# Kernel tuning notes

Measured on AMD Instinct MI355X. Metric: run time of the kernel, lower is better.

## Reference

```python
import jax, jax.numpy as jnp
import numpy as np

B, W, D, R = 8, 1024, 1024, 64
GAMMA_MIN, GAMMA_MAX, ALPHA_CAP, EPS = 0.15, 1.0, 1.0, 1e-8


def _linear_init(key, fan_in, shape):
    bound = 1.0 / np.sqrt(fan_in)
    return jax.random.uniform(key, shape, jnp.float32, -bound, bound)


def setup_inputs() -> dict:
    key = jax.random.key(0)
    ks = jax.random.split(key, 12)
    h = jax.random.normal(ks[0], (B, W, D), jnp.float32)
    # k_base init as in __init__: exp(-0.15*max(j-i,0)) * tril, row-normalized
    pos = jnp.arange(W, dtype=jnp.float32)
    dist_ji = jnp.clip(pos[None, :] - pos[:, None], 0.0)
    causal = jnp.tril(jnp.ones((W, W), jnp.float32))
    k_init = jnp.exp(-0.15 * dist_ji) * causal
    k_base = k_init / jnp.clip(k_init.sum(axis=1, keepdims=True), 1e-8)
    # decay_logit init: gammas in [0.95, 0.995] -> inverse sigmoid of normalized gamma
    gammas = jnp.linspace(0.95, 0.995, R)
    graw = jnp.clip((gammas - GAMMA_MIN) / (GAMMA_MAX - GAMMA_MIN), 1e-6, 1 - 1e-6)
    decay_logit = jnp.log(graw / (1.0 - graw))
    return {
        "h": h,
        "k_base": k_base,
        "decay_logit": decay_logit,
        "gate_logit": jnp.asarray(8.0, jnp.float32),
        "alpha_logit": jnp.asarray(0.0, jnp.float32),
        "u": 0.05 * jax.random.normal(ks[1], (D, R), jnp.float32),
        "v": 0.05 * jax.random.normal(ks[2], (D, R), jnp.float32),
        "proj_w": _linear_init(ks[3], D, (D, D)),
        "proj_b": _linear_init(ks[4], D, (D,)),
        "norm1_scale": jnp.ones((D,), jnp.float32),
        "norm2_scale": jnp.ones((D,), jnp.float32),
        "up_w": _linear_init(ks[5], D, (2 * D, D)),
        "up_b": _linear_init(ks[6], D, (2 * D,)),
        "down_w": _linear_init(ks[7], 2 * D, (D, 2 * D)),
        "down_b": _linear_init(ks[8], 2 * D, (D,)),
    }


def _rmsnorm(x, scale):
    return x * jax.lax.rsqrt(jnp.mean(x * x, axis=-1, keepdims=True) + 1e-8) * scale


def _l2norm(x):
    # mirrors F.normalize(x, dim=-1, eps=1e-8)
    n = jnp.sqrt(jnp.sum(x * x, axis=-1, keepdims=True))
    return x / jnp.maximum(n, EPS)


def reference(h, k_base, decay_logit, gate_logit, alpha_logit, u, v,
              proj_w, proj_b, norm1_scale, norm2_scale,
              up_w, up_b, down_w, down_b):
    _, w, _ = h.shape
    pos = jnp.arange(w, dtype=h.dtype)
    causal = jnp.tril(jnp.ones((w, w), h.dtype))          # [W, W]
    dist = jnp.clip(pos[:, None] - pos[None, :], 0.0)     # i - j, clamped >= 0

    residual = h
    h_norm = _rmsnorm(h, norm1_scale)

    # dense k_base path (k_base_rank == 0)
    gate = jax.nn.sigmoid(gate_logit)
    kb = k_base[:w, :w] * causal
    out = gate * jnp.einsum('ij,bjd->bid', kb, h_norm)

    # low-rank q/k with per-rank gamma decay (decay_impl='mask')
    qk = h_norm @ jnp.concatenate((u, v), axis=1)          # [B, W, 2R]
    q_raw, k_raw = jnp.split(qk, [u.shape[1]], axis=-1)
    q = _l2norm(q_raw)
    k = _l2norm(k_raw)

    gamma = GAMMA_MIN + (GAMMA_MAX - GAMMA_MIN) * jax.nn.sigmoid(decay_logit)  # [R]
    log_gamma = jnp.log(jnp.clip(gamma, 1e-8))
    decay_mask = jnp.exp(dist[:, :, None] * log_gamma[None, None, :]) * causal[:, :, None]  # [W, W, R]

    alpha = ALPHA_CAP * jax.nn.sigmoid(alpha_logit)
    # scores[b,i,j] = sum_r q[b,i,r] * decay[i,j,r] * k[b,j,r]
    scores = jnp.einsum('bir,ijr,bjr->bij', q, decay_mask, k)
    out = out + alpha * jnp.einsum('bij,bjd->bid', scores, h_norm)

    h1 = residual + (out @ proj_w.T + proj_b)
    # MLP (GELU exact, mult=2), second residual
    m = _rmsnorm(h1, norm2_scale)
    m = jax.nn.gelu(m @ up_w.T + up_b, approximate=False) @ down_w.T + down_b
    return h1 + m
```

## Files before the change

kernel.cpp:

```cpp
#include <hip/hip_runtime.h>
#include <hip/hip_bf16.h>
#include <math.h>

#define B_ 8
#define W_ 1024
#define D_ 1024
#define R_ 64

typedef __hip_bfloat16 bf16;
typedef __attribute__((ext_vector_type(8))) short bf16x8;
typedef __attribute__((ext_vector_type(4))) float f32x4;

__device__ __forceinline__ float tof(bf16 x) { return __bfloat162float(x); }
__device__ __forceinline__ short f2bs(float f) {
    bf16 b = __float2bfloat16(f);
    return *(short*)&b;
}

__device__ __forceinline__ void async16(const void* g, void* l) {
    __builtin_amdgcn_global_load_lds(
        (const __attribute__((address_space(1))) unsigned int*)g,
        (__attribute__((address_space(3))) unsigned int*)l,
        16, 0, 0);
}

__global__ __launch_bounds__(256)
void rmsnorm_kernel(const float* __restrict__ src, const float* __restrict__ scale,
                    bf16* __restrict__ dst) {
    int row = blockIdx.x;
    const float* x = src + (size_t)row * D_;
    bf16* y = dst + (size_t)row * D_;
    float xv[4];
    float ss = 0.f;
#pragma unroll
    for (int it = 0; it < 4; ++it) {
        int d = threadIdx.x + it * 256;
        xv[it] = x[d];
        ss += xv[it] * xv[it];
    }
#pragma unroll
    for (int off = 32; off; off >>= 1) ss += __shfl_down(ss, off, 64);
    __shared__ float red[4];
    __shared__ float invs;
    int lane = threadIdx.x & 63, wid = threadIdx.x >> 6;
    if (lane == 0) red[wid] = ss;
    __syncthreads();
    if (threadIdx.x == 0) {
        float t = red[0] + red[1] + red[2] + red[3];
        invs = rsqrtf(t / (float)D_ + 1e-8f);
    }
    __syncthreads();
    float inv = invs;
#pragma unroll
    for (int it = 0; it < 4; ++it) {
        int d = threadIdx.x + it * 256;
        y[d] = __float2bfloat16(xv[it] * inv * scale[d]);
    }
}

__global__ __launch_bounds__(256)
void transpose_kernel(const bf16* __restrict__ src, bf16* __restrict__ dst) {
    int b = blockIdx.z;
    int j0 = blockIdx.x * 64, d0 = blockIdx.y * 64;
    __shared__ short Ts[64][72];
    const bf16* S = src + (size_t)b * W_ * D_;
    bf16* Dd = dst + (size_t)b * W_ * D_;
    int tid = threadIdx.x;
    int r = tid >> 3, c = (tid & 7) * 8;
#pragma unroll
    for (int p = 0; p < 2; ++p) {
        int j = r + p * 32;
        bf16x8 vv = *(const bf16x8*)&S[(size_t)(j0 + j) * D_ + d0 + c];
#pragma unroll
        for (int e = 0; e < 8; ++e) Ts[j][c + e] = vv[e];
    }
    __syncthreads();
#pragma unroll
    for (int p = 0; p < 2; ++p) {
        int d = r + p * 32;
        bf16x8 vv;
#pragma unroll
        for (int e = 0; e < 8; ++e) vv[e] = Ts[c + e][d];
        *(bf16x8*)&Dd[(size_t)(d0 + d) * W_ + j0 + c] = vv;
    }
}

__global__ __launch_bounds__(256)
void uvT_kernel(const float* __restrict__ u, const float* __restrict__ v,
                bf16* __restrict__ uvT) {
    int g = blockIdx.z;
    int d0 = blockIdx.x * 64;
    const float* src = g ? v : u;
    __shared__ float Ts[64][65];
    int tid = threadIdx.x;
#pragma unroll
    for (int e = 0; e < 16; ++e) {
        int idx = tid + e * 256;
        int drow = idx >> 6, rcol = idx & 63;
        Ts[drow][rcol] = src[(size_t)(d0 + drow) * 64 + rcol];
    }
    __syncthreads();
#pragma unroll
    for (int e = 0; e < 16; ++e) {
        int idx = tid + e * 256;
        int orow = idx >> 6, ocol = idx & 63;
        uvT[(size_t)(g * 64 + orow) * D_ + d0 + ocol] = __float2bfloat16(Ts[ocol][orow]);
    }
}

__global__ __launch_bounds__(256)
void convert3_kernel(const float* __restrict__ proj, const float* __restrict__ up,
                     const float* __restrict__ down,
                     bf16* __restrict__ projb, bf16* __restrict__ upb,
                     bf16* __restrict__ downb) {
    size_t idx = ((size_t)blockIdx.x * 256 + threadIdx.x) * 8;
    const size_t DD = (size_t)D_ * D_;
    const float* src; bf16* dst; size_t off;
    if (idx < DD)          { src = proj; dst = projb; off = idx; }
    else if (idx < 3 * DD) { src = up;   dst = upb;   off = idx - DD; }
    else                   { src = down; dst = downb; off = idx - 3 * DD; }
    float4 f0 = *(const float4*)(src + off);
    float4 f1 = *(const float4*)(src + off + 4);
    bf16x8 p;
    p[0] = f2bs(f0.x); p[1] = f2bs(f0.y); p[2] = f2bs(f0.z); p[3] = f2bs(f0.w);
    p[4] = f2bs(f1.x); p[5] = f2bs(f1.y); p[6] = f2bs(f1.z); p[7] = f2bs(f1.w);
    *(bf16x8*)(dst + off) = p;
}

__global__ __launch_bounds__(128)
void qk_epilogue_kernel(const float* __restrict__ qkraw,
                        const float* __restrict__ decay_logit,
                        float* __restrict__ qg, float* __restrict__ kg) {
    int row = blockIdx.x;
    int i = row & (W_ - 1);
    int t = threadIdx.x;
    int r = t & 63;
    bool isK = t >= 64;
    const size_t PS = (size_t)B_ * W_ * 128;
    size_t off = (size_t)row * 128 + t;
    float val = qkraw[off] + qkraw[PS + off] + qkraw[2 * PS + off] + qkraw[3 * PS + off];
    float sq = val * val;
#pragma unroll
    for (int o = 32; o; o >>= 1) sq += __shfl_xor(sq, o, 64);
    val = val / fmaxf(sqrtf(sq), 1e-8f);

    float dl = decay_logit[r];
    float gamma = 0.15f + 0.85f * (1.f / (1.f + expf(-dl)));
    float lg = logf(gamma);
    float e = isK ? expf(-(float)i * lg) : expf((float)i * lg);
    float o = val * e;
    if (isK) kg[(size_t)row * R_ + r] = o;
    else     qg[(size_t)row * R_ + r] = o;
}

__global__ __launch_bounds__(256)
void buildM_kernel(const float* __restrict__ qg, const float* __restrict__ kg,
                   const float* __restrict__ k_base,
                   const float* __restrict__ gate_logit,
                   const float* __restrict__ alpha_logit,
                   bf16* __restrict__ M) {
    int b = blockIdx.z;
    int ti = blockIdx.y, tj = blockIdx.x;
    int i0 = ti * 32, j0 = tj * 32;
    int tx = threadIdx.x, ty = threadIdx.y;
    bf16* Mb = M + (size_t)b * W_ * W_;
    const bf16 zero = __float2bfloat16(0.f);

    if (tj > ti) {
#pragma unroll
        for (int a = 0; a < 2; ++a)
#pragma unroll
            for (int c = 0; c < 2; ++c)
                Mb[(size_t)(i0 + ty * 2 + a) * W_ + (j0 + tx * 2 + c)] = zero;
        return;
    }

    __shared__ float Qs[32][65];
    __shared__ float Ks[32][65];
    int tid = ty * 16 + tx;
    for (int e = tid; e < 32 * 64; e += 256) {
        int rr = e & 63, row = e >> 6;
        Qs[row][rr] = qg[((size_t)b * W_ + i0 + row) * R_ + rr];
        Ks[row][rr] = kg[((size_t)b * W_ + j0 + row) * R_ + rr];
    }
    __syncthreads();

    float acc[2][2] = {{0.f, 0.f}, {0.f, 0.f}};
#pragma unroll 8
    for (int r = 0; r < 64; ++r) {
        float qa = Qs[ty * 2 + 0][r], qb = Qs[ty * 2 + 1][r];
        float ka = Ks[tx * 2 + 0][r], kb = Ks[tx * 2 + 1][r];
        acc[0][0] += qa * ka; acc[0][1] += qa * kb;
        acc[1][0] += qb * ka; acc[1][1] += qb * kb;
    }

    float gate  = 1.f / (1.f + expf(-(*gate_logit)));
    float alpha = 1.f / (1.f + expf(-(*alpha_logit)));
#pragma unroll
    for (int a = 0; a < 2; ++a) {
#pragma unroll
        for (int c = 0; c < 2; ++c) {
            int i = i0 + ty * 2 + a, j = j0 + tx * 2 + c;
            float vkb = k_base[(size_t)i * W_ + j];
            float out = (j <= i) ? (gate * vkb + alpha * acc[a][c]) : 0.f;
            Mb[(size_t)i * W_ + j] = __float2bfloat16(out);
        }
    }
}

#define BAR() do { __builtin_amdgcn_sched_barrier(0); \
                   __builtin_amdgcn_s_barrier(); \
                   __builtin_amdgcn_sched_barrier(0); } while (0)

__device__ __forceinline__ void mfma8(const bf16x8 (&fa)[2], const bf16x8 (&fb)[4],
                                      f32x4 (&acc)[2][4]) {
#pragma unroll
    for (int mi = 0; mi < 2; ++mi)
#pragma unroll
        for (int ni = 0; ni < 4; ++ni)
            acc[mi][ni] = __builtin_amdgcn_mfma_f32_16x16x32_bf16(
                fa[mi], fb[ni], acc[mi][ni], 0, 0, 0);
}

__device__ __forceinline__ void readf(const short* At0, const short* Bt0, int slot,
                                      const int (&ao)[2], const int (&bo)[4],
                                      bf16x8 (&fa)[2], bf16x8 (&fb)[4]) {
    const short* Ard = At0 + slot * 4096;
    const short* Brd = Bt0 + slot * 4096;
#pragma unroll
    for (int mi = 0; mi < 2; ++mi) fa[mi] = *(const bf16x8*)&Ard[ao[mi]];
#pragma unroll
    for (int ni = 0; ni < 4; ++ni) fb[ni] = *(const bf16x8*)&Brd[bo[ni]];
}

__device__ __forceinline__ void mfma16(const bf16x8 (&fa)[4], const bf16x8 (&fb)[4],
                                       f32x4 (&acc)[4][4]) {
#pragma unroll
    for (int mi = 0; mi < 4; ++mi)
#pragma unroll
        for (int ni = 0; ni < 4; ++ni)
            acc[mi][ni] = __builtin_amdgcn_mfma_f32_16x16x32_bf16(
                fa[mi], fb[ni], acc[mi][ni], 0, 0, 0);
}

__device__ __forceinline__ void readf4(const short* At0, const short* Bt0, int slot,
                                       const int (&ao)[4], const int (&bo)[4],
                                       bf16x8 (&fa)[4], bf16x8 (&fb)[4]) {
    const short* Ard = At0 + slot * 4096;
    const short* Brd = Bt0 + slot * 4096;
#pragma unroll
    for (int mi = 0; mi < 4; ++mi) fa[mi] = *(const bf16x8*)&Ard[ao[mi]];
#pragma unroll
    for (int ni = 0; ni < 4; ++ni) fb[ni] = *(const bf16x8*)&Brd[bo[ni]];
}

template<int EPI, int SK>
__global__ __launch_bounds__(512, 4)
void mgemm_kernel(const bf16* __restrict__ A, const bf16* __restrict__ Bm,
                  const float* __restrict__ Res, const float* __restrict__ bias,
                  void* __restrict__ Cout,
                  int M, int N, int K,
                  long sA, long sB, long sC, int causal) {
    __shared__ __align__(16) short At[5][128 * 32];
    __shared__ __align__(16) short Bt[5][128 * 32];
    int z = blockIdx.z;
    const bf16* Ab = (SK > 1) ? A : A + (size_t)z * sA;
    const bf16* Bb = (SK > 1) ? Bm : Bm + (size_t)z * sB;
    int kchunk = K / SK;
    int kbeg = (SK > 1) ? z * kchunk : 0;
    int m0 = blockIdx.x * 128, n0 = blockIdx.y * 128;
    int tid = threadIdx.x;
    int lane = tid & 63, wave = tid >> 6;
    int wy = wave >> 1, wx = wave & 1;
    int quad = lane >> 4, l15 = lane & 15;

    f32x4 acc[2][4];
#pragma unroll
    for (int i = 0; i < 2; ++i)
#pragma unroll
        for (int j = 0; j < 4; ++j)
            acc[i][j] = (f32x4){0.f, 0.f, 0.f, 0.f};

    int kend = kbeg + kchunk;
    if (SK == 1 && causal) kend = (m0 + 128 < K) ? m0 + 128 : K;
    int nIter = (kend - kbeg) >> 5;

    int srcChunk = ((lane & 3) ^ ((lane >> 3) & 3)) * 8;
    size_t rowA = (size_t)(m0 + wave * 16 + (lane >> 2)) * K;
    size_t rowB = (size_t)(n0 + wave * 16 + (lane >> 2)) * K;
    const bf16* aP = Ab + rowA + srcChunk + kbeg;
    const bf16* bP = Bb + rowB + srcChunk + kbeg;
    short* aDst = &At[0][0] + wave * 512;
    short* bDst = &Bt[0][0] + wave * 512;

    int rswz = (quad ^ ((l15 >> 1) & 3)) * 8;
    int ao[2], bo[4];
#pragma unroll
    for (int mi = 0; mi < 2; ++mi) ao[mi] = (wy * 32 + mi * 16 + l15) * 32 + rswz;
#pragma unroll
    for (int ni = 0; ni < 4; ++ni) bo[ni] = (wx * 64 + ni * 16 + l15) * 32 + rswz;

#pragma unroll
    for (int p = 0; p < 4; ++p) {
        async16(aP, aDst + p * 4096);
        async16(bP, bDst + p * 4096);
        aP += 32; bP += 32;
    }
    asm volatile("s_waitcnt vmcnt(6)" ::: "memory");
    BAR();

    bf16x8 fa0[2], fb0[4], fa1[2], fb1[4];
    readf(&At[0][0], &Bt[0][0], 0, ao, bo, fa0, fb0);

    int sStage = 4;
    int sPf = 1;
    int nMain = nIter - 4;

    for (int t = 0; t < nMain; t += 2) {
        asm volatile("s_waitcnt vmcnt(4)" ::: "memory");
        BAR();
        async16(aP, aDst + sStage * 4096);
        async16(bP, bDst + sStage * 4096);
        aP += 32; bP += 32;
        sStage = (sStage == 4) ? 0 : sStage + 1;
        mfma8(fa0, fb0, acc);
        readf(&At[0][0], &Bt[0][0], sPf, ao, bo, fa1, fb1);
        sPf = (sPf == 4) ? 0 : sPf + 1;
        asm volatile("s_waitcnt vmcnt(4)" ::: "memory");
        BAR();
        async16(aP, aDst + sStage * 4096);
        async16(bP, bDst + sStage * 4096);
        aP += 32; bP += 32;
        sStage = (sStage == 4) ? 0 : sStage + 1;
        mfma8(fa1, fb1, acc);
        readf(&At[0][0], &Bt[0][0], sPf, ao, bo, fa0, fb0);
        sPf = (sPf == 4) ? 0 : sPf + 1;
    }

    asm volatile("s_waitcnt vmcnt(4)" ::: "memory");
    BAR();
    mfma8(fa0, fb0, acc);
    readf(&At[0][0], &Bt[0][0], sPf, ao, bo, fa1, fb1);
    sPf = (sPf == 4) ? 0 : sPf + 1;

    asm volatile("s_waitcnt vmcnt(2)" ::: "memory");
    BAR();
    mfma8(fa1, fb1, acc);
    readf(&At[0][0], &Bt[0][0], sPf, ao, bo, fa0, fb0);
    sPf = (sPf == 4) ? 0 : sPf + 1;

    asm volatile("s_waitcnt vmcnt(0)" ::: "memory");
    BAR();
    mfma8(fa0, fb0, acc);
    readf(&At[0][0], &Bt[0][0], sPf, ao, bo, fa1, fb1);

    mfma8(fa1, fb1, acc);

#pragma unroll
    for (int ni = 0; ni < 4; ++ni) {
        int col = n0 + wx * 64 + ni * 16 + l15;
        float bv = (EPI == 1 || EPI == 2) ? bias[col] : 0.f;
#pragma unroll
        for (int mi = 0; mi < 2; ++mi) {
            int row0 = m0 + wy * 32 + mi * 16 + quad * 4;
#pragma unroll
            for (int r = 0; r < 4; ++r) {
                size_t idx = (size_t)(row0 + r) * N + col;
                float val = acc[mi][ni][r];
                if constexpr (EPI == 0) {
                    ((bf16*)Cout)[(size_t)z * sC + idx] = __float2bfloat16(val);
                } else if constexpr (EPI == 1) {
                    ((float*)Cout)[idx] = val + bv + Res[idx];
                } else if constexpr (EPI == 2) {
                    val += bv;
                    val = 0.5f * val * (1.f + erff(val * 0.70710678118654752f));
                    ((bf16*)Cout)[idx] = __float2bfloat16(val);
                } else {
                    ((float*)Cout)[(size_t)z * sC + idx] = val;
                }
            }
        }
    }
}

template<int EPI>
__global__ __launch_bounds__(256, 2)
void mgemm3_kernel(const bf16* __restrict__ A, const bf16* __restrict__ Bm,
                   const float* __restrict__ Res, const float* __restrict__ bias,
                   void* __restrict__ Cout,
                   int M, int N, int K, long sA, long sB, long sC, int causal) {
    __shared__ __align__(16) short At[4][128 * 32];
    __shared__ __align__(16) short Bt[4][128 * 32];
    int z = blockIdx.z;
    const bf16* Ab = A + (size_t)z * sA;
    const bf16* Bb = Bm + (size_t)z * sB;

    int bx = blockIdx.x, gx = gridDim.x;
    if ((gx & 7) == 0) { int cpx = gx >> 3; bx = (bx & 7) * cpx + (bx >> 3); }
    int m0 = bx * 128, n0 = blockIdx.y * 128;

    int tid = threadIdx.x;
    int lane = tid & 63, wave = tid >> 6;
    int wm = wave >> 1, wn = wave & 1;
    int quad = lane >> 4, l15 = lane & 15;

    f32x4 acc[4][4];
#pragma unroll
    for (int i = 0; i < 4; ++i)
#pragma unroll
        for (int j = 0; j < 4; ++j)
            acc[i][j] = (f32x4){0.f, 0.f, 0.f, 0.f};

    int kend = causal ? ((m0 + 128 < K) ? m0 + 128 : K) : K;
    int nIter = kend >> 5;

    int srcChunk = ((lane & 3) ^ ((lane >> 3) & 3)) * 8;
    const bf16* aP0 = Ab + (size_t)(m0 + wave * 32 + (lane >> 2)) * K + srcChunk;
    const bf16* aP1 = aP0 + (size_t)16 * K;
    const bf16* bP0 = Bb + (size_t)(n0 + wave * 32 + (lane >> 2)) * K + srcChunk;
    const bf16* bP1 = bP0 + (size_t)16 * K;
    short* aDst = &At[0][0] + wave * 1024;
    short* bDst = &Bt[0][0] + wave * 1024;

    int rswz = (quad ^ ((l15 >> 1) & 3)) * 8;
    int ao[4], bo[4];
#pragma unroll
    for (int mi = 0; mi < 4; ++mi) ao[mi] = (wm * 64 + mi * 16 + l15) * 32 + rswz;
#pragma unroll
    for (int ni = 0; ni < 4; ++ni) bo[ni] = (wn * 64 + ni * 16 + l15) * 32 + rswz;

#define STG3(slot) do { \
        short* _a = aDst + (slot) * 4096; \
        short* _b = bDst + (slot) * 4096; \
        async16(aP0, _a); async16(aP1, _a + 512); \
        async16(bP0, _b); async16(bP1, _b + 512); \
        aP0 += 32; aP1 += 32; bP0 += 32; bP1 += 32; \
    } while (0)

    STG3(0); STG3(1); STG3(2);
    asm volatile("s_waitcnt vmcnt(8)" ::: "memory");
    BAR();

    bf16x8 fa0[4], fb0[4], fa1[4], fb1[4];
    readf4(&At[0][0], &Bt[0][0], 0, ao, bo, fa0, fb0);

    int sStage = 3;
    int sPf = 1;
    int nMain = nIter - 2;

    for (int t = 0; t < nMain; t += 2) {
        asm volatile("s_waitcnt vmcnt(4)" ::: "memory");
        BAR();
        if (t + 3 < nIter) { STG3(sStage & 3); ++sStage; }
        mfma16(fa0, fb0, acc);
        readf4(&At[0][0], &Bt[0][0], sPf & 3, ao, bo, fa1, fb1);
        ++sPf;
        if (t + 3 < nIter) asm volatile("s_waitcnt vmcnt(4)" ::: "memory");
        else               asm volatile("s_waitcnt vmcnt(0)" ::: "memory");
        BAR();
        if (t + 4 < nIter) { STG3(sStage & 3); ++sStage; }
        mfma16(fa1, fb1, acc);
        readf4(&At[0][0], &Bt[0][0], sPf & 3, ao, bo, fa0, fb0);
        ++sPf;
    }

    asm volatile("s_waitcnt vmcnt(0)" ::: "memory");
    BAR();
    mfma16(fa0, fb0, acc);
    readf4(&At[0][0], &Bt[0][0], sPf & 3, ao, bo, fa1, fb1);
    mfma16(fa1, fb1, acc);
#undef STG3

#pragma unroll
    for (int ni = 0; ni < 4; ++ni) {
        int col = n0 + wn * 64 + ni * 16 + l15;
        float bv = (EPI == 1 || EPI == 2) ? bias[col] : 0.f;
#pragma unroll
        for (int mi = 0; mi < 4; ++mi) {
            int row0 = m0 + wm * 64 + mi * 16 + quad * 4;
#pragma unroll
            for (int r = 0; r < 4; ++r) {
                size_t idx = (size_t)(row0 + r) * N + col;
                float val = acc[mi][ni][r];
                if constexpr (EPI == 0) {
                    ((bf16*)Cout)[(size_t)z * sC + idx] = __float2bfloat16(val);
                } else if constexpr (EPI == 1) {
                    ((float*)Cout)[idx] = val + bv + Res[idx];
                } else {
                    val += bv;
                    val = 0.5f * val * (1.f + erff(val * 0.70710678118654752f));
                    ((bf16*)Cout)[idx] = __float2bfloat16(val);
                }
            }
        }
    }
}

extern "C" void kernel_launch(void* const* d_in, const int* in_sizes, int n_in,
                              void* d_out, int out_size, void* d_ws, size_t ws_size,
                              hipStream_t stream) {
    const float* h           = (const float*)d_in[0];
    const float* k_base      = (const float*)d_in[1];
    const float* decay_logit = (const float*)d_in[2];
    const float* gate_logit  = (const float*)d_in[3];
    const float* alpha_logit = (const float*)d_in[4];
    const float* u           = (const float*)d_in[5];
    const float* v           = (const float*)d_in[6];
    const float* proj_w      = (const float*)d_in[7];
    const float* proj_b      = (const float*)d_in[8];
    const float* norm1_scale = (const float*)d_in[9];
    const float* norm2_scale = (const float*)d_in[10];
    const float* up_w        = (const float*)d_in[11];
    const float* up_b        = (const float*)d_in[12];
    const float* down_w      = (const float*)d_in[13];
    const float* down_b      = (const float*)d_in[14];

    const size_t MB = 1048576;
    char* ws = (char*)d_ws;
    bf16*  hnorm   = (bf16*)(ws);
    bf16*  uvT     = (bf16*)(ws + 16 * MB);
    float* qg      = (float*)(ws + 16 * MB);
    float* kg      = (float*)(ws + 18 * MB);
    bf16*  hnormT  = (bf16*)(ws + 20 * MB);
    float* qkraw   = (float*)(ws + 36 * MB);
    bf16*  Mbuf    = (bf16*)(ws + 36 * MB);
    bf16*  proj_wb = (bf16*)(ws + 52 * MB);
    bf16*  up_wb   = (bf16*)(ws + 54 * MB);
    bf16*  down_wb = (bf16*)(ws + 58 * MB);
    bf16*  attn    = hnorm;
    bf16*  mnorm   = hnorm;
    bf16*  tbuf    = hnormT;
    float* h1      = (float*)d_out;

    convert3_kernel<<<5 * D_ * D_ / 2048, 256, 0, stream>>>(
        proj_w, up_w, down_w, proj_wb, up_wb, down_wb);
    uvT_kernel<<<dim3(D_ / 64, 1, 2), 256, 0, stream>>>(u, v, uvT);

    rmsnorm_kernel<<<B_ * W_, 256, 0, stream>>>(h, norm1_scale, hnorm);

    transpose_kernel<<<dim3(W_ / 64, D_ / 64, B_), 256, 0, stream>>>(hnorm, hnormT);

    mgemm_kernel<5, 4><<<dim3(B_ * W_ / 128, 1, 4), 512, 0, stream>>>(
        hnorm, uvT, nullptr, nullptr, qkraw, B_ * W_, 128, D_,
        0, 0, (long)B_ * W_ * 128, 0);

    qk_epilogue_kernel<<<B_ * W_, 128, 0, stream>>>(qkraw, decay_logit, qg, kg);

    buildM_kernel<<<dim3(W_ / 32, W_ / 32, B_), dim3(16, 16), 0, stream>>>(
        qg, kg, k_base, gate_logit, alpha_logit, Mbuf);

    mgemm3_kernel<0><<<dim3(W_ / 128, D_ / 128, B_), 256, 0, stream>>>(
        Mbuf, hnormT, nullptr, nullptr, attn, W_, D_, W_,
        (long)W_ * W_, (long)W_ * D_, (long)W_ * D_, 1);

    mgemm3_kernel<1><<<dim3(B_ * W_ / 128, D_ / 128, 1), 256, 0, stream>>>(
        attn, proj_wb, h, proj_b, h1, B_ * W_, D_, D_, 0, 0, 0, 0);

    rmsnorm_kernel<<<B_ * W_, 256, 0, stream>>>(h1, norm2_scale, mnorm);

    mgemm3_kernel<2><<<dim3(B_ * W_ / 128, 2 * D_ / 128, 1), 256, 0, stream>>>(
        mnorm, up_wb, nullptr, up_b, tbuf, B_ * W_, 2 * D_, D_, 0, 0, 0, 0);

    mgemm3_kernel<1><<<dim3(B_ * W_ / 128, D_ / 128, 1), 256, 0, stream>>>(
        tbuf, down_wb, h1, down_b, (float*)d_out, B_ * W_, D_, 2 * D_, 0, 0, 0, 0);
}
```

Before: 356.3 us.

## Use a three-stage LDS ring in the GEMM to fit three blocks per CU

The shared-memory pipeline of the main GEMM kernel shrinks from four to three stages, and the launch bound goes from 2 to 3 blocks per CU to raise occupancy. The loop is reordered so each async global-to-LDS copy is issued before the vmcnt wait and barrier. An explicit lgkmcnt(0) wait plus a scheduling barrier now follows each fragment read. This trades prefetch depth and some compiler scheduling freedom for more resident waves. Tighter register limits could cause spills, and slot reuse now relies on the new wait ordering.

```diff
diff --git a/kernel.cpp b/kernel.cpp
--- a/kernel.cpp
+++ b/kernel.cpp
@@ -384,13 +384,13 @@
 }
 
 template<int EPI>
-__global__ __launch_bounds__(256, 2)
-void mgemm3_kernel(const bf16* __restrict__ A, const bf16* __restrict__ Bm,
+__global__ __launch_bounds__(256, 3)
+void mgemm4_kernel(const bf16* __restrict__ A, const bf16* __restrict__ Bm,
                    const float* __restrict__ Res, const float* __restrict__ bias,
                    void* __restrict__ Cout,
                    int M, int N, int K, long sA, long sB, long sC, int causal) {
-    __shared__ __align__(16) short At[4][128 * 32];
-    __shared__ __align__(16) short Bt[4][128 * 32];
+    __shared__ __align__(16) short At[3][128 * 32];
+    __shared__ __align__(16) short Bt[3][128 * 32];
     int z = blockIdx.z;
     const bf16* Ab = A + (size_t)z * sA;
     const bf16* Bb = Bm + (size_t)z * sB;
@@ -436,40 +436,45 @@
         async16(bP0, _b); async16(bP1, _b + 512); \
         aP0 += 32; aP1 += 32; bP0 += 32; bP1 += 32; \
     } while (0)
-
-    STG3(0); STG3(1); STG3(2);
-    asm volatile("s_waitcnt vmcnt(8)" ::: "memory");
+#define LGKM0() do { asm volatile("s_waitcnt lgkmcnt(0)" ::: "memory"); \
+                     __builtin_amdgcn_sched_barrier(0); } while (0)
+
+    STG3(0); STG3(1);
+    asm volatile("s_waitcnt vmcnt(4)" ::: "memory");
     BAR();
 
     bf16x8 fa0[4], fb0[4], fa1[4], fb1[4];
     readf4(&At[0][0], &Bt[0][0], 0, ao, bo, fa0, fb0);
-
-    int sStage = 3;
+    LGKM0();
+
+    int sStage = 2;
     int sPf = 1;
     int nMain = nIter - 2;
 
     for (int t = 0; t < nMain; t += 2) {
+        STG3(sStage); sStage = (sStage == 2) ? 0 : sStage + 1;
         asm volatile("s_waitcnt vmcnt(4)" ::: "memory");
         BAR();
-        if (t + 3 < nIter) { STG3(sStage & 3); ++sStage; }
         mfma16(fa0, fb0, acc);
-        readf4(&At[0][0], &Bt[0][0], sPf & 3, ao, bo, fa1, fb1);
-        ++sPf;
-        if (t + 3 < nIter) asm volatile("s_waitcnt vmcnt(4)" ::: "memory");
-        else               asm volatile("s_waitcnt vmcnt(0)" ::: "memory");
+        readf4(&At[0][0], &Bt[0][0], sPf, ao, bo, fa1, fb1);
+        sPf = (sPf == 2) ? 0 : sPf + 1;
+        LGKM0();
+        STG3(sStage); sStage = (sStage == 2) ? 0 : sStage + 1;
+        asm volatile("s_waitcnt vmcnt(4)" ::: "memory");
         BAR();
-        if (t + 4 < nIter) { STG3(sStage & 3); ++sStage; }
         mfma16(fa1, fb1, acc);
-        readf4(&At[0][0], &Bt[0][0], sPf & 3, ao, bo, fa0, fb0);
-        ++sPf;
+        readf4(&At[0][0], &Bt[0][0], sPf, ao, bo, fa0, fb0);
+        sPf = (sPf == 2) ? 0 : sPf + 1;
+        LGKM0();
     }
 
     asm volatile("s_waitcnt vmcnt(0)" ::: "memory");
     BAR();
     mfma16(fa0, fb0, acc);
-    readf4(&At[0][0], &Bt[0][0], sPf & 3, ao, bo, fa1, fb1);
+    readf4(&At[0][0], &Bt[0][0], sPf, ao, bo, fa1, fb1);
     mfma16(fa1, fb1, acc);
 #undef STG3
+#undef LGKM0
 
 #pragma unroll
     for (int ni = 0; ni < 4; ++ni) {
@@ -549,18 +554,18 @@
     buildM_kernel<<<dim3(W_ / 32, W_ / 32, B_), dim3(16, 16), 0, stream>>>(
         qg, kg, k_base, gate_logit, alpha_logit, Mbuf);
 
-    mgemm3_kernel<0><<<dim3(W_ / 128, D_ / 128, B_), 256, 0, stream>>>(
+    mgemm4_kernel<0><<<dim3(W_ / 128, D_ / 128, B_), 256, 0, stream>>>(
         Mbuf, hnormT, nullptr, nullptr, attn, W_, D_, W_,
         (long)W_ * W_, (long)W_ * D_, (long)W_ * D_, 1);
 
-    mgemm3_kernel<1><<<dim3(B_ * W_ / 128, D_ / 128, 1), 256, 0, stream>>>(
+    mgemm4_kernel<1><<<dim3(B_ * W_ / 128, D_ / 128, 1), 256, 0, stream>>>(
         attn, proj_wb, h, proj_b, h1, B_ * W_, D_, D_, 0, 0, 0, 0);
 
     rmsnorm_kernel<<<B_ * W_, 256, 0, stream>>>(h1, norm2_scale, mnorm);
 
-    mgemm3_kernel<2><<<dim3(B_ * W_ / 128, 2 * D_ / 128, 1), 256, 0, stream>>>(
+    mgemm4_kernel<2><<<dim3(B_ * W_ / 128, 2 * D_ / 128, 1), 256, 0, stream>>>(
         mnorm, up_wb, nullptr, up_b, tbuf, B_ * W_, 2 * D_, D_, 0, 0, 0, 0);
 
-    mgemm3_kernel<1><<<dim3(B_ * W_ / 128, D_ / 128, 1), 256, 0, stream>>>(
+    mgemm4_kernel<1><<<dim3(B_ * W_ / 128, D_ / 128, 1), 256, 0, stream>>>(
         tbuf, down_wb, h1, down_b, (float*)d_out, B_ * W_, D_, 2 * D_, 0, 0, 0, 0);
 }
```

Result: no change. 351.1 us (-1.5%).
